# Performance work log

Measured on AMD Instinct MI355X. Metric: run time of the kernel, lower is better.

The kernel has to match this reference:

```python
import jax, jax.numpy as jnp
import numpy as np
import math

N = 32768
C = 128
K = 16
CHUNK = 2048
LN_EPS = float(C)  # original code calls torch.nn.LayerNorm(C, C): second positional arg is eps -> eps = 128.0 (faithful)


def knn_idx(coords):
    """Brute-force KNN on full coords [N,4] (matches knn_points(x_C, x_C, K=16)), chunked over queries."""
    def one_chunk(q):  # q: [CHUNK,4]
        d = jnp.sum((q[:, None, :] - coords[None, :, :]) ** 2, axis=-1)  # [CHUNK,N]
        return jax.lax.top_k(-d, K)[1]  # ascending distance (return_sorted=True)
    qs = coords.reshape(-1, CHUNK, coords.shape[-1])
    return jax.lax.map(one_chunk, qs).reshape(-1, K)  # [N,K]


def layer_norm(x, g, b):
    mu = jnp.mean(x, axis=-1, keepdims=True)
    var = jnp.mean((x - mu) ** 2, axis=-1, keepdims=True)
    return (x - mu) / jnp.sqrt(var + LN_EPS) * g + b


def self_attention(x_f, xyz_enc, new_feature, qw, qb, kw, kb, vw, vb):
    Q = x_f @ qw + qb                              # [N,C]
    nf = new_feature + xyz_enc                     # [N,K,C]
    Kt = nf @ kw + kb                              # [N,K,C]
    scores = jnp.einsum('nkd,nd->nk', Kt, Q) / math.sqrt(C)
    a = jax.nn.softmax(scores, axis=-1)            # [N,K]
    V = nf @ vw + vb                               # [N,K,C]
    return jnp.einsum('nk,nkd->nd', a, V)          # [N,C]


def setup_inputs() -> dict:
    key = jax.random.key(0)
    ks = jax.random.split(key, 22)
    xyz = jax.random.uniform(ks[0], (N, 3), dtype=jnp.float32) * 100.0
    coords = jnp.concatenate([jnp.zeros((N, 1), jnp.float32), xyz], axis=1)  # [N,4] batch col = 0
    feats = jax.random.normal(ks[1], (N, C), dtype=jnp.float32)
    s = 0.02
    def lin(k, din, dout):
        kw, kb = jax.random.split(k)
        return jax.random.normal(kw, (din, dout), jnp.float32) * s, jax.random.normal(kb, (dout,), jnp.float32) * s
    pos_w, pos_b = lin(ks[2], 3, C)
    pos1_w, pos1_b = lin(ks[3], 3, C)
    qw0, qb0 = lin(ks[4], C, C); kw0, kb0 = lin(ks[5], C, C); vw0, vb0 = lin(ks[6], C, C)
    qw1, qb1 = lin(ks[7], C, C); kw1, kb1 = lin(ks[8], C, C); vw1, vb1 = lin(ks[9], C, C)
    lin_w, lin_b = lin(ks[10], C, C)  # MinkowskiConvolution kernel_size=1 == pointwise linear
    return {
        'coords': coords, 'feats': feats,
        'pos_w': pos_w, 'pos_b': pos_b, 'pos1_w': pos1_w, 'pos1_b': pos1_b,
        'qw0': qw0, 'qb0': qb0, 'kw0': kw0, 'kb0': kb0, 'vw0': vw0, 'vb0': vb0,
        'qw1': qw1, 'qb1': qb1, 'kw1': kw1, 'kb1': kb1, 'vw1': vw1, 'vb1': vb1,
        'lin_w': lin_w, 'lin_b': lin_b,
        'g0': jnp.ones((C,), jnp.float32), 'be0': jnp.zeros((C,), jnp.float32),
        'g1': jnp.ones((C,), jnp.float32), 'be1': jnp.zeros((C,), jnp.float32),
    }


def reference(coords, feats, pos_w, pos_b, pos1_w, pos1_b,
              qw0, qb0, kw0, kb0, vw0, vb0,
              qw1, qb1, kw1, kb1, vw1, vb1,
              lin_w, lin_b, g0, be0, g1, be1):
    idx = knn_idx(coords)                           # [N,K]
    xyz = coords[:, 1:]                             # [N,3]
    new_xyz = xyz[:, None, :] - xyz[idx]            # [N,K,3] relative offsets
    # block 1
    xyz_enc = new_xyz @ pos_w + pos_b               # [N,K,C]
    nf = feats[idx]                                 # gather [N,K,C]
    o = self_attention(feats, xyz_enc, nf, qw0, qb0, kw0, kb0, vw0, vb0)
    # block 2: re-gather updated features with same idx
    nf1 = o[idx]
    xyz_enc1 = new_xyz @ pos1_w + pos1_b
    o = self_attention(o, xyz_enc1, nf1, qw1, qb1, kw1, kb1, vw1, vb1)
    # residual + LN, pointwise conv, residual + LN
    h = layer_norm(feats + o, g0, be0)
    h1 = h @ lin_w + lin_b
    return layer_norm(h + h1, g1, be1)
```

## Files before the change

### kernel.cpp

```cpp
#include <hip/hip_runtime.h>
#include <stdint.h>

#define NPT 32768

typedef unsigned int u32;
typedef unsigned short u16;
typedef unsigned long long u64;

typedef short v8s __attribute__((ext_vector_type(8)));
typedef float v4f __attribute__((ext_vector_type(4)));

__device__ __forceinline__ float b2f(u16 u) {
  union { u32 u; float f; } x; x.u = ((u32)u) << 16; return x.f;
}
__device__ __forceinline__ u16 f2b(float f) {
  union { float f; u32 u; } x; x.f = f;
  u32 u = x.u;
  return (u16)((u + 0x7fffu + ((u >> 16) & 1u)) >> 16);
}
__device__ __forceinline__ bool probe_f32(const void* coords) {
  return ((const u16*)coords)[1] == 0;
}
__device__ __forceinline__ float ldany(const void* p, long i, bool f32) {
  return f32 ? ((const float*)p)[i] : b2f(((const u16*)p)[i]);
}
__device__ __forceinline__ float wsum(float v) {
#pragma unroll
  for (int m = 1; m < 64; m <<= 1) v += __shfl_xor(v, m, 64);
  return v;
}
__device__ __forceinline__ v8s ldA8(const void* feats, long row, int off, bool f32) {
  union { uint4 u; v8s s; } c;
  if (f32) {
    const float* f = (const float*)feats + row * 128 + off;
    float4 x = *(const float4*)f;
    float4 y = *(const float4*)(f + 4);
    c.u.x = (u32)f2b(x.x) | ((u32)f2b(x.y) << 16);
    c.u.y = (u32)f2b(x.z) | ((u32)f2b(x.w) << 16);
    c.u.z = (u32)f2b(y.x) | ((u32)f2b(y.y) << 16);
    c.u.w = (u32)f2b(y.z) | ((u32)f2b(y.w) << 16);
  } else {
    c.u = *(const uint4*)((const u16*)feats + row * 128 + off);
  }
  return c.s;
}

#define GC 16
#define GH 6.25f
#define GINV 0.16f
#define NCELL (GC * GC * GC)

__device__ __forceinline__ int cell1d(float v) {
  int c = (int)(v * GINV);
  return c > (GC - 1) ? (GC - 1) : (c < 0 ? 0 : c);
}

__global__ __launch_bounds__(256) void grid_scan(int* __restrict__ cellStart, int* __restrict__ cellPtr) {
  __shared__ int part[256];
  const int t = threadIdx.x;
  int local[16]; int s = 0;
#pragma unroll
  for (int i = 0; i < 16; i++) { local[i] = cellStart[1 + t * 16 + i]; s += local[i]; }
  part[t] = s;
  __syncthreads();
  for (int off = 1; off < 256; off <<= 1) {
    int v = (t >= off) ? part[t - off] : 0;
    __syncthreads();
    part[t] += v;
    __syncthreads();
  }
  int run = (t == 0) ? 0 : part[t - 1];
#pragma unroll
  for (int i = 0; i < 16; i++) {
    int c = t * 16 + i;
    cellPtr[c] = run;
    run += local[i];
    cellStart[c + 1] = run;
  }
}

__global__ __launch_bounds__(256) void grid_scatter(const float* __restrict__ cx, const float* __restrict__ cy,
                                                    const float* __restrict__ cz, const int* __restrict__ pcell,
                                                    int* __restrict__ cellPtr, float4* __restrict__ sortedP,
                                                    int* __restrict__ rank) {
  int i = blockIdx.x * 256 + threadIdx.x;
  int c = pcell[i];
  int pos = atomicAdd(&cellPtr[c], 1);
  sortedP[pos] = make_float4(cx[i], cy[i], cz[i], __int_as_float(i));
  rank[i] = pos;
}

__device__ __forceinline__ void knn_body(int blk, int tid,
                                         const float4* __restrict__ sortedP,
                                         const int* __restrict__ cellStart,
                                         const int* __restrict__ rank,
                                         u16* __restrict__ idxout) {
  const int lane = tid & 63;
  const int gl = lane & 15;
  const int grp = lane >> 4;
  const int q = blk * 16 + (tid >> 4);
  const float4 p = sortedP[q];
  const float qx = p.x, qy = p.y, qz = p.z;
  const int qcx = cell1d(qx), qcy = cell1d(qy), qcz = cell1d(qz);
  const float fx = qx - qcx * GH, fy = qy - qcy * GH, fz = qz - qcz * GH;

  u64 R = ~0ull;
  u64 k15v = ~0ull;

  auto key_of = [&](int g) -> u64 {
    float4 sp = sortedP[g];
    float dx = __fsub_rn(qx, sp.x), dy = __fsub_rn(qy, sp.y), dzc = __fsub_rn(qz, sp.z);
    float d = __fadd_rn(__fadd_rn(__fmul_rn(dx, dx), __fmul_rn(dy, dy)), __fmul_rn(dzc, dzc));
    return ((u64)__float_as_uint(d) << 32) | (u32)__float_as_int(sp.w);
  };

  auto shfl64 = [&](u64 v, int s) -> u64 {
    int lo = __shfl((int)(u32)v, s, 16);
    int hi = __shfl((int)(u32)(v >> 32), s, 16);
    return ((u64)(u32)hi << 32) | (u32)lo;
  };
  auto sxg = [&](u64 v, int m) -> u64 {
    int lo = __shfl_xor((int)(u32)v, m, 64);
    int hi = __shfl_xor((int)(u32)(v >> 32), m, 64);
    return ((u64)(u32)hi << 32) | (u32)lo;
  };
  auto upg = [&](u64 v) -> u64 {
    int lo = __shfl_up((int)(u32)v, 1, 16);
    int hi = __shfl_up((int)(u32)(v >> 32), 1, 16);
    return ((u64)(u32)hi << 32) | (u32)lo;
  };

  auto insert_one = [&](u64 kk) {
    u64 prev = upg(R);
    if (gl == 0) prev = 0ull;
    R = (kk < R) ? ((kk >= prev) ? kk : prev) : R;
  };

  auto batch_merge = [&](u64 key) {
    u64 mask = __ballot(key < k15v);
    u32 mymask = (u32)((mask >> (grp * 16)) & 0xffffu);
    if (mymask == 0) return;
    int pcount = __popc(mymask);
    if (pcount <= 8) {
      u32 mm = mymask;
      while (mm) {
        int s = __ffs((int)mm) - 1;
        mm &= mm - 1;
        insert_one(shfl64(key, s));
      }
      k15v = shfl64(R, 15);
      return;
    }
#pragma unroll
    for (int k = 2; k <= 16; k <<= 1) {
#pragma unroll
      for (int j = k >> 1; j > 0; j >>= 1) {
        u64 o = sxg(key, j);
        bool up = ((gl & k) == 0);
        bool lower = ((gl & j) == 0);
        u64 mn = key < o ? key : o;
        u64 mx = key < o ? o : key;
        key = (lower == up) ? mn : mx;
      }
    }
    u64 s = sxg(key, 15);
    u64 mn = R < s ? R : s;
#pragma unroll
    for (int j = 8; j > 0; j >>= 1) {
      u64 o = sxg(mn, j);
      bool lower = ((gl & j) == 0);
      u64 lo = mn < o ? mn : o;
      u64 hi = mn < o ? o : mn;
      mn = lower ? lo : hi;
    }
    R = mn;
    k15v = shfl64(R, 15);
  };

  auto scan_range_grp = [&](int s0, int s1) {
    if (s0 >= s1) return;
    int g0 = s0 + gl;
    u64 key = (g0 < s1) ? key_of(g0) : ~0ull;
    for (int base = s0; base < s1; base += 16) {
      int gn = base + 16 + gl;
      u64 nkey = (base + 16 < s1) ? ((gn < s1) ? key_of(gn) : ~0ull) : ~0ull;
      batch_merge(key);
      key = nkey;
    }
  };

  {
    const int xlo = qcx - 1 < 0 ? 0 : qcx - 1;
    const int xhi = qcx + 1 > GC - 1 ? GC - 1 : qcx + 1;
    {
      int rb = (qcz * GC + qcy) * GC;
      scan_range_grp(cellStart[rb + xlo], cellStart[rb + xhi + 1]);
    }
    const int rdz[8] = { 0, 0, -1, 1, -1, -1, 1, 1 };
    const int rdy[8] = { -1, 1, 0, 0, -1, 1, -1, 1 };
#pragma unroll
    for (int s_ = 0; s_ < 8; s_++) {
      int dz = rdz[s_], dy = rdy[s_];
      int z = qcz + dz, y = qcy + dy;
      if (z < 0 || z > GC - 1 || y < 0 || y > GC - 1) continue;
      float gz = (dz == 0) ? 0.f : (dz < 0 ? fz : GH - fz);
      float gy = (dy == 0) ? 0.f : (dy < 0 ? fy : GH - fy);
      float rowb = gz * gz + gy * gy;
      float d15 = __uint_as_float((u32)(k15v >> 32));
      if (d15 < rowb * 0.998f - 1e-4f) continue;
      int rb = (z * GC + y) * GC;
      scan_range_grp(cellStart[rb + xlo], cellStart[rb + xhi + 1]);
    }
  }

  auto ubound = [&](int rr) -> float {
    float b = 1e30f;
    if (qcx - rr - 1 >= 0) b = fminf(b, fx + rr * GH);
    if (qcx + rr + 1 <= GC - 1) b = fminf(b, (rr + 1) * GH - fx);
    if (qcy - rr - 1 >= 0) b = fminf(b, fy + rr * GH);
    if (qcy + rr + 1 <= GC - 1) b = fminf(b, (rr + 1) * GH - fy);
    if (qcz - rr - 1 >= 0) b = fminf(b, fz + rr * GH);
    if (qcz + rr + 1 <= GC - 1) b = fminf(b, (rr + 1) * GH - fz);
    return b;
  };

  {
    float d15 = __uint_as_float((u32)(k15v >> 32));
    float b1 = ubound(1);
    bool done = (b1 > 1e29f) || (d15 < b1 * b1 * 0.998f - 1e-4f);
    if (!done) {
      for (int r = 2; r < GC; ++r) {
        int zlo = qcz - r < 0 ? 0 : qcz - r, zhi = qcz + r > GC - 1 ? GC - 1 : qcz + r;
        for (int z = zlo; z <= zhi; ++z) {
          int adz = z - qcz; adz = adz < 0 ? -adz : adz;
          bool ez = (adz == r);
          int ylo = qcy - r < 0 ? 0 : qcy - r, yhi = qcy + r > GC - 1 ? GC - 1 : qcy + r;
          for (int y = ylo; y <= yhi; ++y) {
            int ady = y - qcy; ady = ady < 0 ? -ady : ady;
            bool ey = (ady == r);
            int rb = (z * GC + y) * GC;
            if (ez || ey) {
              int xlo = qcx - r < 0 ? 0 : qcx - r, xhi = qcx + r > GC - 1 ? GC - 1 : qcx + r;
              scan_range_grp(cellStart[rb + xlo], cellStart[rb + xhi + 1]);
            } else {
              int xm = qcx - r, xp = qcx + r;
              if (xm >= 0) scan_range_grp(cellStart[rb + xm], cellStart[rb + xm + 1]);
              if (xp <= GC - 1) scan_range_grp(cellStart[rb + xp], cellStart[rb + xp + 1]);
            }
          }
        }
        float d15b = __uint_as_float((u32)(k15v >> 32));
        float b = ubound(r);
        if (b > 1e29f || d15b < b * b * 0.998f - 1e-4f) break;
      }
    }
  }

  idxout[(size_t)q * 16 + gl] = (u16)rank[(int)(u32)R];
}

__device__ __forceinline__ void gemm_body(int blk, int tid, const void* coords,
                                          const u16* __restrict__ A, const void* __restrict__ featsAny,
                                          const float4* __restrict__ sortedPtr,
                                          const u16* __restrict__ Bf, const void* __restrict__ bias,
                                          u16* __restrict__ Qb, u16* __restrict__ KVb,
                                          const float* __restrict__ tblp, float* __restrict__ pOut,
                                          int ntiles) {
  const bool f32 = probe_f32(coords);
  const int lane = tid & 63;
  const int wave = tid >> 6;
  const int r0 = blk * 64 + wave * 16;
  const int quad = lane >> 4, lr = lane & 15;
  v8s a[4];
  if (sortedPtr) {
    long arow = (long)__float_as_int(sortedPtr[r0 + lr].w);
#pragma unroll
    for (int kq = 0; kq < 4; kq++) a[kq] = ldA8(featsAny, arow, kq * 32 + quad * 8, f32);
  } else {
#pragma unroll
    for (int kq = 0; kq < 4; kq++) {
      union { uint4 u; v8s s; } c;
      c.u = *(const uint4*)(A + (size_t)(r0 + lr) * 128 + kq * 32 + quad * 8);
      a[kq] = c.s;
    }
  }
  float pd0[4] = { 0.f, 0.f, 0.f, 0.f };
  float pd1[4] = { 0.f, 0.f, 0.f, 0.f };
  float pd2[4] = { 0.f, 0.f, 0.f, 0.f };
  float pd3[4] = { 0.f, 0.f, 0.f, 0.f };
  for (int tile = 0; tile < ntiles; ++tile) {
    v4f acc = { 0.f, 0.f, 0.f, 0.f };
#pragma unroll
    for (int kq = 0; kq < 4; kq++) {
      union { uint4 u; v8s s; } c;
      c.u = *(const uint4*)(Bf + ((size_t)(tile * 4 + kq) * 64 + lane) * 8);
      acc = __builtin_amdgcn_mfma_f32_16x16x32_bf16(a[kq], c.s, acc, 0, 0, 0);
    }
    int col = tile * 16 + lr;
    if (col < 128) {
      float bb = ldany(bias, col, f32);
      float t0 = tblp[col], t1 = tblp[128 + col], t2 = tblp[256 + col], t3 = tblp[768 + col];
#pragma unroll
      for (int r = 0; r < 4; r++) {
        float qv = acc[r] + bb;
        Qb[(size_t)(r0 + quad * 4 + r) * 128 + col] = f2b(qv);
        pd0[r] += t0 * qv;
        pd1[r] += t1 * qv;
        pd2[r] += t2 * qv;
        pd3[r] += t3 * qv;
      }
    } else {
#pragma unroll
      for (int r = 0; r < 4; r++) KVb[(size_t)(r0 + quad * 4 + r) * 256 + (col - 128)] = f2b(acc[r]);
    }
  }
  {
#pragma unroll
    for (int m = 1; m < 16; m <<= 1) {
#pragma unroll
      for (int r = 0; r < 4; r++) {
        pd0[r] += __shfl_xor(pd0[r], m, 64);
        pd1[r] += __shfl_xor(pd1[r], m, 64);
        pd2[r] += __shfl_xor(pd2[r], m, 64);
        pd3[r] += __shfl_xor(pd3[r], m, 64);
      }
    }
    if (lr < 4) {
#pragma unroll
      for (int r = 0; r < 4; r++) {
        float v = (lr == 0) ? pd0[r] : ((lr == 1) ? pd1[r] : ((lr == 2) ? pd2[r] : pd3[r]));
        pOut[(size_t)(r0 + quad * 4 + r) * 4 + lr] = v;
      }
    }
  }
}

__global__ __launch_bounds__(256) void knn_gemm0(const float4* __restrict__ sortedP,
                                                 const int* __restrict__ cellStart,
                                                 const int* __restrict__ rank,
                                                 u16* __restrict__ idxout,
                                                 const void* __restrict__ coords,
                                                 const void* __restrict__ feats,
                                                 const u16* __restrict__ Bf, const void* __restrict__ bias,
                                                 u16* __restrict__ Qb, u16* __restrict__ KVb,
                                                 const float* __restrict__ tblp, float* __restrict__ pOut) {
  if (blockIdx.x < 2048) {
    knn_body(blockIdx.x, threadIdx.x, sortedP, cellStart, rank, idxout);
  } else {
    gemm_body(blockIdx.x - 2048, threadIdx.x, coords, (const u16*)nullptr, feats, sortedP,
              Bf, bias, Qb, KVb, tblp, pOut, 24);
  }
}

__global__ __launch_bounds__(256) void gemm_kernel(const void* __restrict__ coords,
                                                   const u16* __restrict__ A, const u16* __restrict__ Bf,
                                                   const void* __restrict__ bias, u16* __restrict__ Qb,
                                                   u16* __restrict__ KVb,
                                                   const float* __restrict__ tblp, float* __restrict__ pOut,
                                                   int ntiles) {
  gemm_body(blockIdx.x, threadIdx.x, coords, A, (const void*)nullptr, (const float4*)nullptr,
            Bf, bias, Qb, KVb, tblp, pOut, ntiles);
}

__global__ __launch_bounds__(256) void gemm_ln(const void* __restrict__ coords,
                                               const u16* __restrict__ A ,
                                               const u16* __restrict__ Bf, const void* __restrict__ bias,
                                               const float4* __restrict__ sortedP,
                                               const void* __restrict__ g, const void* __restrict__ be,
                                               void* __restrict__ outAny) {
  const bool f32 = probe_f32(coords);
  const int lane = threadIdx.x & 63;
  const int wave = threadIdx.x >> 6;
  const int r0 = blockIdx.x * 64 + wave * 16;
  const int quad = lane >> 4, lr = lane & 15;
  v8s a[4];
#pragma unroll
  for (int kq = 0; kq < 4; kq++) {
    union { uint4 u; v8s s; } c;
    c.u = *(const uint4*)(A + (size_t)(r0 + lr) * 128 + kq * 32 + quad * 8);
    a[kq] = c.s;
  }
  float xv[8][4];
#pragma unroll
  for (int tile = 0; tile < 8; ++tile) {
    v4f acc = { 0.f, 0.f, 0.f, 0.f };
#pragma unroll
    for (int kq = 0; kq < 4; kq++) {
      union { uint4 u; v8s s; } c;
      c.u = *(const uint4*)(Bf + ((size_t)(tile * 4 + kq) * 64 + lane) * 8);
      acc = __builtin_amdgcn_mfma_f32_16x16x32_bf16(a[kq], c.s, acc, 0, 0, 0);
    }
    int col = tile * 16 + lr;
    float bb = ldany(bias, col, f32);
#pragma unroll
    for (int r = 0; r < 4; r++) {
      float h = b2f(A[(size_t)(r0 + quad * 4 + r) * 128 + col]);
      xv[tile][r] = h + acc[r] + bb;
    }
  }
  float sum[4];
#pragma unroll
  for (int r = 0; r < 4; r++) {
    sum[r] = 0.f;
#pragma unroll
    for (int tile = 0; tile < 8; ++tile) sum[r] += xv[tile][r];
  }
#pragma unroll
  for (int m = 1; m < 16; m <<= 1) {
#pragma unroll
    for (int r = 0; r < 4; r++) sum[r] += __shfl_xor(sum[r], m, 64);
  }
  float mu[4];
#pragma unroll
  for (int r = 0; r < 4; r++) mu[r] = sum[r] * (1.f / 128.f);
  float vs[4];
#pragma unroll
  for (int r = 0; r < 4; r++) {
    vs[r] = 0.f;
#pragma unroll
    for (int tile = 0; tile < 8; ++tile) {
      float d = xv[tile][r] - mu[r];
      vs[r] += d * d;
    }
  }
#pragma unroll
  for (int m = 1; m < 16; m <<= 1) {
#pragma unroll
    for (int r = 0; r < 4; r++) vs[r] += __shfl_xor(vs[r], m, 64);
  }
  float rinv[4];
#pragma unroll
  for (int r = 0; r < 4; r++) rinv[r] = 1.0f / sqrtf(vs[r] * (1.f / 128.f) + 128.0f);
  long orig[4];
#pragma unroll
  for (int r = 0; r < 4; r++) orig[r] = (long)__float_as_int(sortedP[r0 + quad * 4 + r].w);
#pragma unroll
  for (int tile = 0; tile < 8; ++tile) {
    int col = tile * 16 + lr;
    float gv = ldany(g, col, f32), bv = ldany(be, col, f32);
#pragma unroll
    for (int r = 0; r < 4; r++) {
      float y = (xv[tile][r] - mu[r]) * rinv[r] * gv + bv;
      if (f32) ((float*)outAny)[orig[r] * 128 + col] = y;
      else ((u16*)outAny)[orig[r] * 128 + col] = f2b(y);
    }
  }
}

__global__ __launch_bounds__(256) void prep_all(
    const void* coords,
    const void* pw0, const void* pb0, const void* kw0, const void* kb0, const void* vw0, const void* vb0,
    const void* pw1, const void* pb1, const void* kw1, const void* kb1, const void* vw1, const void* vb1,
    float* __restrict__ tbl, int* __restrict__ cellStart,
    float* __restrict__ cx, float* __restrict__ cy, float* __restrict__ cz, int* __restrict__ pcell,
    const void* __restrict__ qw0, const void* __restrict__ qw1, const void* __restrict__ linw,
    u16* __restrict__ Bf0, u16* __restrict__ Bf1, u16* __restrict__ BfL) {
  const bool f32 = probe_f32(coords);
  if (blockIdx.x < 512) {
    const int lane = threadIdx.x & 63;
    const int o = blockIdx.x * 4 + (threadIdx.x >> 6);
    const int l = o >> 10;
    const int rem = o & 1023;
    const void* PW = l ? pw1 : pw0;
    const void* PB = l ? pb1 : pb0;
    const void* KW = l ? kw1 : kw0;
    const void* KB = l ? kb1 : kb0;
    const void* VW = l ? vw1 : vw0;
    const void* VB = l ? vb1 : vb0;
    float acc, extra = 0.f;
    if (rem < 768) {
      bool isV = rem >= 384;
      int r2 = isV ? rem - 384 : rem;
      int i = r2 >> 7, c = r2 & 127;
      const void* W = isV ? VW : KW;
      acc = ldany(PW, i * 128 + lane, f32) * ldany(W, (long)lane * 128 + c, f32)
          + ldany(PW, i * 128 + lane + 64, f32) * ldany(W, (long)(lane + 64) * 128 + c, f32);
    } else {
      bool isV = rem >= 896;
      int c = rem & 127;
      const void* W = isV ? VW : KW;
      const void* B = isV ? VB : KB;
      acc = ldany(PB, lane, f32) * ldany(W, (long)lane * 128 + c, f32)
          + ldany(PB, lane + 64, f32) * ldany(W, (long)(lane + 64) * 128 + c, f32);
      extra = ldany(B, c, f32);
    }
    acc = wsum(acc) + extra;
    if (lane == 0) tbl[l * 1024 + rem] = acc;
  } else if (blockIdx.x < 640) {
    int i = (blockIdx.x - 512) * 256 + threadIdx.x;
    float x = ldany(coords, (long)i * 4 + 1, f32);
    float y = ldany(coords, (long)i * 4 + 2, f32);
    float z = ldany(coords, (long)i * 4 + 3, f32);
    cx[i] = x; cy[i] = y; cz[i] = z;
    int c = (cell1d(z) * GC + cell1d(y)) * GC + cell1d(x);
    pcell[i] = c;
    atomicAdd(&cellStart[c + 1], 1);
  } else {
    int tid = (blockIdx.x - 640) * 256 + threadIdx.x;
    const void *w0, *w1, *w2; u16* out; int t;
    if (tid < 49152) { t = tid; w0 = qw0; w1 = kw0; w2 = vw0; out = Bf0; }
    else if (tid < 98304) { t = tid - 49152; w0 = qw1; w1 = kw1; w2 = vw1; out = Bf1; }
    else { t = tid - 98304; w0 = linw; w1 = linw; w2 = linw; out = BfL; }
    int j = t & 7, lane = (t >> 3) & 63, kq = (t >> 9) & 3, tile = t >> 11;
    int k = kq * 32 + ((lane >> 4) << 3) + j;
    int col = tile * 16 + (lane & 15);
    const void* w = (col < 128) ? w0 : ((col < 256) ? w1 : w2);
    long off = (long)k * 128 + (col & 127);
    out[t] = f32 ? f2b(((const float*)w)[off]) : ((const u16*)w)[off];
  }
}

__global__ __launch_bounds__(256) void attn_kernel(const void* __restrict__ coordsRaw,
                                                   const float4* __restrict__ sortedP,
                                                   const u16* __restrict__ idx,
                                                   const u16* __restrict__ Qb, const u16* __restrict__ KVb,
                                                   const float* __restrict__ tbl, const float* __restrict__ p4,
                                                   const void* __restrict__ feats,
                                                   const void* __restrict__ g, const void* __restrict__ be,
                                                   u16* __restrict__ outB, int mode) {
  const int lane = threadIdx.x & 63;
  const int swz = (blockIdx.x & 7) * (gridDim.x >> 3) + (blockIdx.x >> 3);
  const int n = swz * 4 + (threadIdx.x >> 6);
  const int c0 = 2 * lane;
  const int k = lane & 15;
  const int quad = lane >> 4;
  const int base = lane & 48;

  const int j = idx[(size_t)n * 16 + k];
  u32 vr[16];
#pragma unroll
  for (int k2 = 0; k2 < 16; k2++) {
    int jk = __shfl(j, base + k2, 64);
    vr[k2] = *(const u32*)(KVb + (size_t)jk * 256 + 128 + c0);
  }
  uint4 kf[4];
#pragma unroll
  for (int kq = 0; kq < 4; kq++) {
    kf[kq] = *(const uint4*)(KVb + (size_t)j * 256 + kq * 32 + quad * 8);
  }
  const float4 P = sortedP[n];
  const float4 Pj = sortedP[j];
  const float nx = P.x - Pj.x, ny = P.y - Pj.y, nz = P.z - Pj.z;
  const float4 pv = *(const float4*)(p4 + (size_t)n * 4);

  v4f sacc = { 0.f, 0.f, 0.f, 0.f };
#pragma unroll
  for (int kq = 0; kq < 4; kq++) {
    union { uint4 u; v8s s; } ka, qa;
    ka.u = kf[kq];
    qa.u = *(const uint4*)(Qb + (size_t)n * 128 + kq * 32 + quad * 8);
    sacc = __builtin_amdgcn_mfma_f32_16x16x32_bf16(ka.s, qa.s, sacc, 0, 0, 0);
  }
  const int srcl = ((k >> 2) << 4) | k;
  float t0 = __shfl(sacc[0], srcl, 64);
  float t1 = __shfl(sacc[1], srcl, 64);
  float t2 = __shfl(sacc[2], srcl, 64);
  float t3 = __shfl(sacc[3], srcl, 64);
  float s = (k & 2) ? ((k & 1) ? t3 : t2) : ((k & 1) ? t1 : t0);
  float sc = (s + nx * pv.x + ny * pv.y + nz * pv.z + pv.w) * 0.08838834764831845f;

  float mx = sc;
#pragma unroll
  for (int m = 1; m < 16; m <<= 1) mx = fmaxf(mx, __shfl_xor(mx, m, 64));
  float e = expf(sc - mx);
  float ssum = e;
#pragma unroll
  for (int m = 1; m < 16; m <<= 1) ssum += __shfl_xor(ssum, m, 64);
  const float a = e / ssum;

  float wx = a * nx, wy = a * ny, wz = a * nz;
#pragma unroll
  for (int m = 1; m < 16; m <<= 1) {
    wx += __shfl_xor(wx, m, 64);
    wy += __shfl_xor(wy, m, 64);
    wz += __shfl_xor(wz, m, 64);
  }

  float a0 = 0.f, a1 = 0.f;
#pragma unroll
  for (int k2 = 0; k2 < 16; k2++) {
    float ak = __shfl(a, base + k2, 64);
    u32 u = vr[k2];
    a0 += ak * b2f((u16)(u & 0xffffu));
    a1 += ak * b2f((u16)(u >> 16));
  }
  float o0 = a0 + wx * tbl[384 + c0] + wy * tbl[512 + c0] + wz * tbl[640 + c0] + tbl[896 + c0];
  float o1 = a1 + wx * tbl[384 + c0 + 1] + wy * tbl[512 + c0 + 1] + wz * tbl[640 + c0 + 1] + tbl[896 + c0 + 1];
  if (mode == 1) {
    const bool f32 = probe_f32(coordsRaw);
    long orig = (long)__float_as_int(P.w);
    float x0 = ldany(feats, orig * 128 + c0, f32) + o0;
    float x1 = ldany(feats, orig * 128 + c0 + 1, f32) + o1;
    float mu = wsum(x0 + x1) * (1.f / 128.f);
    float d0 = x0 - mu, d1 = x1 - mu;
    float var = wsum(d0 * d0 + d1 * d1) * (1.f / 128.f);
    float rinv = 1.0f / sqrtf(var + 128.0f);
    o0 = d0 * rinv * ldany(g, c0, f32) + ldany(be, c0, f32);
    o1 = d1 * rinv * ldany(g, c0 + 1, f32) + ldany(be, c0 + 1, f32);
  }
  ((u32*)outB)[(size_t)n * 64 + lane] = (u32)f2b(o0) | ((u32)f2b(o1) << 16);
}

extern "C" void kernel_launch(void* const* d_in, const int* in_sizes, int n_in,
                              void* d_out, int out_size, void* d_ws, size_t ws_size,
                              hipStream_t stream) {
  (void)in_sizes; (void)n_in; (void)out_size; (void)ws_size;
  const void* coords = d_in[0];
  const void* feats = d_in[1];
  const void* pos_w = d_in[2];
  const void* pos_b = d_in[3];
  const void* pos1_w = d_in[4];
  const void* pos1_b = d_in[5];
  const void* qw0 = d_in[6];
  const void* qb0 = d_in[7];
  const void* kw0 = d_in[8];
  const void* kb0 = d_in[9];
  const void* vw0 = d_in[10];
  const void* vb0 = d_in[11];
  const void* qw1 = d_in[12];
  const void* qb1 = d_in[13];
  const void* kw1 = d_in[14];
  const void* kb1 = d_in[15];
  const void* vw1 = d_in[16];
  const void* vb1 = d_in[17];
  const void* lin_w = d_in[18];
  const void* lin_b = d_in[19];
  const void* g0 = d_in[20];
  const void* be0 = d_in[21];
  const void* g1 = d_in[22];
  const void* be1 = d_in[23];

  char* w = (char*)d_ws;
  u16* idxp = (u16*)(w + 0);
  float4* sortedP = (float4*)(w + 1048576);
  int* rank = (int*)(w + 1572864);
  float* cx = (float*)(w + 1703936);
  float* cy = (float*)(w + 1835008);
  float* cz = (float*)(w + 1966080);
  float* tbl = (float*)(w + 2097152);
  u16* Bf0 = (u16*)(w + 2105344);
  u16* Bf1 = (u16*)(w + 2203648);
  u16* BfL = (u16*)(w + 2301952);
  float* p4 = (float*)(w + 2334720);
  int* cellStart = (int*)(w + 2859008);
  int* cellPtr = (int*)(w + 2875456);
  int* pcell = (int*)(w + 2891840);
  u16* oS = (u16*)(w + 10723328);
  u16* Qb = (u16*)(w + 19111936);
  u16* KVb = (u16*)(w + 27500544);

  hipMemsetAsync(cellStart, 0, (NCELL + 1) * sizeof(int), stream);

  hipLaunchKernelGGL(prep_all, dim3(1088), dim3(256), 0, stream, coords,
                     pos_w, pos_b, kw0, kb0, vw0, vb0, pos1_w, pos1_b, kw1, kb1, vw1, vb1,
                     tbl, cellStart, cx, cy, cz, pcell, qw0, qw1, lin_w, Bf0, Bf1, BfL);

  hipLaunchKernelGGL(grid_scan, dim3(1), dim3(256), 0, stream, cellStart, cellPtr);
  hipLaunchKernelGGL(grid_scatter, dim3(128), dim3(256), 0, stream, cx, cy, cz, pcell, cellPtr, sortedP, rank);

  hipLaunchKernelGGL(knn_gemm0, dim3(2560), dim3(256), 0, stream, sortedP, cellStart, rank, idxp,
                     coords, feats, Bf0, qb0, Qb, KVb, tbl, p4);

  hipLaunchKernelGGL(attn_kernel, dim3(8192), dim3(256), 0, stream, coords, sortedP, idxp, Qb, KVb, tbl, p4,
                     (const void*)nullptr, (const void*)nullptr, (const void*)nullptr, oS, 0);
  hipLaunchKernelGGL(gemm_kernel, dim3(512), dim3(256), 0, stream, coords, oS, Bf1, qb1, Qb, KVb,
                     tbl + 1024, p4, 24);
  hipLaunchKernelGGL(attn_kernel, dim3(8192), dim3(256), 0, stream, coords, sortedP, idxp, Qb, KVb, tbl + 1024, p4,
                     feats, g0, be0, oS, 1);
  hipLaunchKernelGGL(gemm_ln, dim3(512), dim3(256), 0, stream, coords, oS, BfL, lin_b, sortedP, g1, be1, d_out);
}
```

Measured before the change: 280.1 us.

## Fuse second attention block with pointwise linear and final LayerNorm

Merges the second attention pass (with residual+LN0) and the final gemm_ln kernel into one kernel. Each 4-wave block writes its 4 normalized rows to shared memory, then wave 0 runs the 128x128 linear via MFMA on a 16-row tile padded with zeros, adds the residual, applies LN1 and scatters to the output. This removes one launch and the round trip of the intermediate through global memory. In exchange it wastes 3/4 of the MFMA rows, adds a block barrier, and leaves three waves idle during the GEMM tail.

```diff
diff --git a/kernel.cpp b/kernel.cpp
--- a/kernel.cpp
+++ b/kernel.cpp
@@ -360,91 +360,6 @@
                                                    int ntiles) {
   gemm_body(blockIdx.x, threadIdx.x, coords, A, (const void*)nullptr, (const float4*)nullptr,
             Bf, bias, Qb, KVb, tblp, pOut, ntiles);
-}
-
-__global__ __launch_bounds__(256) void gemm_ln(const void* __restrict__ coords,
-                                               const u16* __restrict__ A ,
-                                               const u16* __restrict__ Bf, const void* __restrict__ bias,
-                                               const float4* __restrict__ sortedP,
-                                               const void* __restrict__ g, const void* __restrict__ be,
-                                               void* __restrict__ outAny) {
-  const bool f32 = probe_f32(coords);
-  const int lane = threadIdx.x & 63;
-  const int wave = threadIdx.x >> 6;
-  const int r0 = blockIdx.x * 64 + wave * 16;
-  const int quad = lane >> 4, lr = lane & 15;
-  v8s a[4];
-#pragma unroll
-  for (int kq = 0; kq < 4; kq++) {
-    union { uint4 u; v8s s; } c;
-    c.u = *(const uint4*)(A + (size_t)(r0 + lr) * 128 + kq * 32 + quad * 8);
-    a[kq] = c.s;
-  }
-  float xv[8][4];
-#pragma unroll
-  for (int tile = 0; tile < 8; ++tile) {
-    v4f acc = { 0.f, 0.f, 0.f, 0.f };
-#pragma unroll
-    for (int kq = 0; kq < 4; kq++) {
-      union { uint4 u; v8s s; } c;
-      c.u = *(const uint4*)(Bf + ((size_t)(tile * 4 + kq) * 64 + lane) * 8);
-      acc = __builtin_amdgcn_mfma_f32_16x16x32_bf16(a[kq], c.s, acc, 0, 0, 0);
-    }
-    int col = tile * 16 + lr;
-    float bb = ldany(bias, col, f32);
-#pragma unroll
-    for (int r = 0; r < 4; r++) {
-      float h = b2f(A[(size_t)(r0 + quad * 4 + r) * 128 + col]);
-      xv[tile][r] = h + acc[r] + bb;
-    }
-  }
-  float sum[4];
-#pragma unroll
-  for (int r = 0; r < 4; r++) {
-    sum[r] = 0.f;
-#pragma unroll
-    for (int tile = 0; tile < 8; ++tile) sum[r] += xv[tile][r];
-  }
-#pragma unroll
-  for (int m = 1; m < 16; m <<= 1) {
-#pragma unroll
-    for (int r = 0; r < 4; r++) sum[r] += __shfl_xor(sum[r], m, 64);
-  }
-  float mu[4];
-#pragma unroll
-  for (int r = 0; r < 4; r++) mu[r] = sum[r] * (1.f / 128.f);
-  float vs[4];
-#pragma unroll
-  for (int r = 0; r < 4; r++) {
-    vs[r] = 0.f;
-#pragma unroll
-    for (int tile = 0; tile < 8; ++tile) {
-      float d = xv[tile][r] - mu[r];
-      vs[r] += d * d;
-    }
-  }
-#pragma unroll
-  for (int m = 1; m < 16; m <<= 1) {
-#pragma unroll
-    for (int r = 0; r < 4; r++) vs[r] += __shfl_xor(vs[r], m, 64);
-  }
-  float rinv[4];
-#pragma unroll
-  for (int r = 0; r < 4; r++) rinv[r] = 1.0f / sqrtf(vs[r] * (1.f / 128.f) + 128.0f);
-  long orig[4];
-#pragma unroll
-  for (int r = 0; r < 4; r++) orig[r] = (long)__float_as_int(sortedP[r0 + quad * 4 + r].w);
-#pragma unroll
-  for (int tile = 0; tile < 8; ++tile) {
-    int col = tile * 16 + lr;
-    float gv = ldany(g, col, f32), bv = ldany(be, col, f32);
-#pragma unroll
-    for (int r = 0; r < 4; r++) {
-      float y = (xv[tile][r] - mu[r]) * rinv[r] * gv + bv;
-      if (f32) ((float*)outAny)[orig[r] * 128 + col] = y;
-      else ((u16*)outAny)[orig[r] * 128 + col] = f2b(y);
-    }
-  }
 }
 
 __global__ __launch_bounds__(256) void prep_all(
@@ -515,9 +430,7 @@
                                                    const u16* __restrict__ idx,
                                                    const u16* __restrict__ Qb, const u16* __restrict__ KVb,
                                                    const float* __restrict__ tbl, const float* __restrict__ p4,
-                                                   const void* __restrict__ feats,
-                                                   const void* __restrict__ g, const void* __restrict__ be,
-                                                   u16* __restrict__ outB, int mode) {
+                                                   u16* __restrict__ outB) {
   const int lane = threadIdx.x & 63;
   const int swz = (blockIdx.x & 7) * (gridDim.x >> 3) + (blockIdx.x >> 3);
   const int n = swz * 4 + (threadIdx.x >> 6);
@@ -586,8 +499,93 @@
   }
   float o0 = a0 + wx * tbl[384 + c0] + wy * tbl[512 + c0] + wz * tbl[640 + c0] + tbl[896 + c0];
   float o1 = a1 + wx * tbl[384 + c0 + 1] + wy * tbl[512 + c0 + 1] + wz * tbl[640 + c0 + 1] + tbl[896 + c0 + 1];
-  if (mode == 1) {
-    const bool f32 = probe_f32(coordsRaw);
+  ((u32*)outB)[(size_t)n * 64 + lane] = (u32)f2b(o0) | ((u32)f2b(o1) << 16);
+}
+
+__global__ __launch_bounds__(256) void attn1_fused(const void* __restrict__ coordsRaw,
+                                                   const float4* __restrict__ sortedP,
+                                                   const u16* __restrict__ idx,
+                                                   const u16* __restrict__ Qb, const u16* __restrict__ KVb,
+                                                   const float* __restrict__ tbl, const float* __restrict__ p4,
+                                                   const void* __restrict__ feats,
+                                                   const void* __restrict__ g0, const void* __restrict__ be0,
+                                                   const u16* __restrict__ BfL, const void* __restrict__ lin_b,
+                                                   const void* __restrict__ g1, const void* __restrict__ be1,
+                                                   void* __restrict__ outAny) {
+  const bool f32 = probe_f32(coordsRaw);
+  const int lane = threadIdx.x & 63;
+  const int wave = threadIdx.x >> 6;
+  const int swz = (blockIdx.x & 7) * (gridDim.x >> 3) + (blockIdx.x >> 3);
+  const int nbase = swz * 4;
+  const int n = nbase + wave;
+  const int c0 = 2 * lane;
+  const int k = lane & 15;
+  const int quad = lane >> 4;
+  const int base = lane & 48;
+
+  __shared__ u32 hlds[256];
+
+  const int j = idx[(size_t)n * 16 + k];
+  u32 vr[16];
+#pragma unroll
+  for (int k2 = 0; k2 < 16; k2++) {
+    int jk = __shfl(j, base + k2, 64);
+    vr[k2] = *(const u32*)(KVb + (size_t)jk * 256 + 128 + c0);
+  }
+  uint4 kf[4];
+#pragma unroll
+  for (int kq = 0; kq < 4; kq++) {
+    kf[kq] = *(const uint4*)(KVb + (size_t)j * 256 + kq * 32 + quad * 8);
+  }
+  const float4 P = sortedP[n];
+  const float4 Pj = sortedP[j];
+  const float nx = P.x - Pj.x, ny = P.y - Pj.y, nz = P.z - Pj.z;
+  const float4 pv = *(const float4*)(p4 + (size_t)n * 4);
+
+  v4f sacc = { 0.f, 0.f, 0.f, 0.f };
+#pragma unroll
+  for (int kq = 0; kq < 4; kq++) {
+    union { uint4 u; v8s s; } ka, qa;
+    ka.u = kf[kq];
+    qa.u = *(const uint4*)(Qb + (size_t)n * 128 + kq * 32 + quad * 8);
+    sacc = __builtin_amdgcn_mfma_f32_16x16x32_bf16(ka.s, qa.s, sacc, 0, 0, 0);
+  }
+  const int srcl = ((k >> 2) << 4) | k;
+  float t0 = __shfl(sacc[0], srcl, 64);
+  float t1 = __shfl(sacc[1], srcl, 64);
+  float t2 = __shfl(sacc[2], srcl, 64);
+  float t3 = __shfl(sacc[3], srcl, 64);
+  float s = (k & 2) ? ((k & 1) ? t3 : t2) : ((k & 1) ? t1 : t0);
+  float sc = (s + nx * pv.x + ny * pv.y + nz * pv.z + pv.w) * 0.08838834764831845f;
+
+  float mx = sc;
+#pragma unroll
+  for (int m = 1; m < 16; m <<= 1) mx = fmaxf(mx, __shfl_xor(mx, m, 64));
+  float e = expf(sc - mx);
+  float ssum = e;
+#pragma unroll
+  for (int m = 1; m < 16; m <<= 1) ssum += __shfl_xor(ssum, m, 64);
+  const float a = e / ssum;
+
+  float wx = a * nx, wy = a * ny, wz = a * nz;
+#pragma unroll
+  for (int m = 1; m < 16; m <<= 1) {
+    wx += __shfl_xor(wx, m, 64);
+    wy += __shfl_xor(wy, m, 64);
+    wz += __shfl_xor(wz, m, 64);
+  }
+
+  float a0 = 0.f, a1 = 0.f;
+#pragma unroll
+  for (int k2 = 0; k2 < 16; k2++) {
+    float ak = __shfl(a, base + k2, 64);
+    u32 u = vr[k2];
+    a0 += ak * b2f((u16)(u & 0xffffu));
+    a1 += ak * b2f((u16)(u >> 16));
+  }
+  float o0 = a0 + wx * tbl[384 + c0] + wy * tbl[512 + c0] + wz * tbl[640 + c0] + tbl[896 + c0];
+  float o1 = a1 + wx * tbl[384 + c0 + 1] + wy * tbl[512 + c0 + 1] + wz * tbl[640 + c0 + 1] + tbl[896 + c0 + 1];
+  {
     long orig = (long)__float_as_int(P.w);
     float x0 = ldany(feats, orig * 128 + c0, f32) + o0;
     float x1 = ldany(feats, orig * 128 + c0 + 1, f32) + o1;
@@ -595,10 +593,94 @@
     float d0 = x0 - mu, d1 = x1 - mu;
     float var = wsum(d0 * d0 + d1 * d1) * (1.f / 128.f);
     float rinv = 1.0f / sqrtf(var + 128.0f);
-    o0 = d0 * rinv * ldany(g, c0, f32) + ldany(be, c0, f32);
-    o1 = d1 * rinv * ldany(g, c0 + 1, f32) + ldany(be, c0 + 1, f32);
-  }
-  ((u32*)outB)[(size_t)n * 64 + lane] = (u32)f2b(o0) | ((u32)f2b(o1) << 16);
+    o0 = d0 * rinv * ldany(g0, c0, f32) + ldany(be0, c0, f32);
+    o1 = d1 * rinv * ldany(g0, c0 + 1, f32) + ldany(be0, c0 + 1, f32);
+  }
+  hlds[wave * 64 + lane] = (u32)f2b(o0) | ((u32)f2b(o1) << 16);
+  __syncthreads();
+  if (wave != 0) return;
+
+  const int lr = lane & 15;
+  v8s a2[4];
+#pragma unroll
+  for (int kq = 0; kq < 4; kq++) {
+    if (lr < 4) {
+      union { uint4 u; v8s s; } c;
+      c.u = *(const uint4*)((const u32*)hlds + lr * 64 + kq * 16 + quad * 4);
+      a2[kq] = c.s;
+    } else {
+      v8s z = { 0, 0, 0, 0, 0, 0, 0, 0 };
+      a2[kq] = z;
+    }
+  }
+  float xv[8][4];
+#pragma unroll
+  for (int tile = 0; tile < 8; ++tile) {
+    v4f acc = { 0.f, 0.f, 0.f, 0.f };
+#pragma unroll
+    for (int kq = 0; kq < 4; kq++) {
+      union { uint4 u; v8s s; } c;
+      c.u = *(const uint4*)(BfL + ((size_t)(tile * 4 + kq) * 64 + lane) * 8);
+      acc = __builtin_amdgcn_mfma_f32_16x16x32_bf16(a2[kq], c.s, acc, 0, 0, 0);
+    }
+    int col = tile * 16 + lr;
+    float bb = ldany(lin_b, col, f32);
+#pragma unroll
+    for (int r = 0; r < 4; r++) {
+      u32 hw = hlds[r * 64 + (tile * 8 + (lr >> 1))];
+      float h = b2f((u16)((hw >> (16 * (lr & 1))) & 0xffffu));
+      xv[tile][r] = h + acc[r] + bb;
+    }
+  }
+  float sum[4];
+#pragma unroll
+  for (int r = 0; r < 4; r++) {
+    sum[r] = 0.f;
+#pragma unroll
+    for (int tile = 0; tile < 8; ++tile) sum[r] += xv[tile][r];
+  }
+#pragma unroll
+  for (int m = 1; m < 16; m <<= 1) {
+#pragma unroll
+    for (int r = 0; r < 4; r++) sum[r] += __shfl_xor(sum[r], m, 64);
+  }
+  float mu[4];
+#pragma unroll
+  for (int r = 0; r < 4; r++) mu[r] = sum[r] * (1.f / 128.f);
+  float vs[4];
+#pragma unroll
+  for (int r = 0; r < 4; r++) {
+    vs[r] = 0.f;
+#pragma unroll
+    for (int tile = 0; tile < 8; ++tile) {
+      float d = xv[tile][r] - mu[r];
+      vs[r] += d * d;
+    }
+  }
+#pragma unroll
+  for (int m = 1; m < 16; m <<= 1) {
+#pragma unroll
+    for (int r = 0; r < 4; r++) vs[r] += __shfl_xor(vs[r], m, 64);
+  }
+  if (quad == 0) {
+    float rinv[4];
+#pragma unroll
+    for (int r = 0; r < 4; r++) rinv[r] = 1.0f / sqrtf(vs[r] * (1.f / 128.f) + 128.0f);
+    long orig[4];
+#pragma unroll
+    for (int r = 0; r < 4; r++) orig[r] = (long)__float_as_int(sortedP[nbase + r].w);
+#pragma unroll
+    for (int tile = 0; tile < 8; ++tile) {
+      int col = tile * 16 + lane;
+      float gv = ldany(g1, col, f32), bv = ldany(be1, col, f32);
+#pragma unroll
+      for (int r = 0; r < 4; r++) {
+        float y = (xv[tile][r] - mu[r]) * rinv[r] * gv + bv;
+        if (f32) ((float*)outAny)[orig[r] * 128 + col] = y;
+        else ((u16*)outAny)[orig[r] * 128 + col] = f2b(y);
+      }
+    }
+  }
 }
 
 extern "C" void kernel_launch(void* const* d_in, const int* in_sizes, int n_in,
@@ -661,11 +743,9 @@
   hipLaunchKernelGGL(knn_gemm0, dim3(2560), dim3(256), 0, stream, sortedP, cellStart, rank, idxp,
                      coords, feats, Bf0, qb0, Qb, KVb, tbl, p4);
 
-  hipLaunchKernelGGL(attn_kernel, dim3(8192), dim3(256), 0, stream, coords, sortedP, idxp, Qb, KVb, tbl, p4,
-                     (const void*)nullptr, (const void*)nullptr, (const void*)nullptr, oS, 0);
+  hipLaunchKernelGGL(attn_kernel, dim3(8192), dim3(256), 0, stream, coords, sortedP, idxp, Qb, KVb, tbl, p4, oS);
   hipLaunchKernelGGL(gemm_kernel, dim3(512), dim3(256), 0, stream, coords, oS, Bf1, qb1, Qb, KVb,
                      tbl + 1024, p4, 24);
-  hipLaunchKernelGGL(attn_kernel, dim3(8192), dim3(256), 0, stream, coords, sortedP, idxp, Qb, KVb, tbl + 1024, p4,
-                     feats, g0, be0, oS, 1);
-  hipLaunchKernelGGL(gemm_ln, dim3(512), dim3(256), 0, stream, coords, oS, BfL, lin_b, sortedP, g1, be1, d_out);
-}
+  hipLaunchKernelGGL(attn1_fused, dim3(8192), dim3(256), 0, stream, coords, sortedP, idxp, Qb, KVb,
+                     tbl + 1024, p4, feats, g0, be0, BfL, lin_b, g1, be1, d_out);
+}
```

Result: slower. 314.2 us (+12.1%).
